# Optimization experiments

Hardware: AMD Instinct MI355X
Metric: run time of the kernel (lower is better)

The kernel has to match this reference:

```python
import jax, jax.numpy as jnp
import numpy as np

DIM_H = 128
HEADS = 8
HEAD_DIM = DIM_H // HEADS
N_NODES = 40000
N_EDGES = 640000
BN_EPS = 1e-5


def setup_inputs() -> dict:
    key = jax.random.key(0)
    ks = jax.random.split(key, 16)
    s = 0.05
    x = jax.random.normal(ks[0], (N_NODES, DIM_H), dtype=jnp.float32)
    edge_index = jax.random.randint(ks[1], (2, N_EDGES), 0, N_NODES, dtype=jnp.int64)
    p = lambda k, shp: jax.random.normal(k, shp, dtype=jnp.float32) * s
    return {
        "x": x,
        "edge_index": edge_index,
        "Wk": p(ks[2], (DIM_H, DIM_H)), "bk": p(ks[3], (DIM_H,)),
        "Wv": p(ks[4], (DIM_H, DIM_H)), "bv": p(ks[5], (DIM_H,)),
        "Wo": p(ks[6], (DIM_H, DIM_H)), "bo": p(ks[7], (DIM_H,)),
        "bn1_g": jnp.ones((DIM_H,), jnp.float32), "bn1_b": jnp.zeros((DIM_H,), jnp.float32),
        "W1": p(ks[8], (2 * DIM_H, DIM_H)), "b1": p(ks[9], (2 * DIM_H,)),
        "W2": p(ks[10], (DIM_H, 2 * DIM_H)), "b2": p(ks[11], (DIM_H,)),
        "bn2_g": jnp.ones((DIM_H,), jnp.float32), "bn2_b": jnp.zeros((DIM_H,), jnp.float32),
    }


def _batchnorm(h, gamma, beta):
    # BatchNorm1d in training mode: per-feature batch mean / biased var over nodes
    mu = jnp.mean(h, axis=0)
    var = jnp.mean((h - mu) ** 2, axis=0)
    return (h - mu) * jax.lax.rsqrt(var + BN_EPS) * gamma + beta


def _sparse_attn(x, edge_index, Wk, bk, Wv, bv, Wo, bo):
    N = x.shape[0]
    src, dst = edge_index[0], edge_index[1]
    K = (x @ Wk.T + bk).reshape(N, HEADS, HEAD_DIM)
    V = (x @ Wv.T + bv).reshape(N, HEADS, HEAD_DIM)
    Q = x.reshape(N, HEADS, HEAD_DIM)  # query is raw h (no projection)
    # per-edge scores [E, H]
    scores = jnp.sum(K[src] * Q[dst], axis=-1) / np.sqrt(HEAD_DIM).astype(np.float32)
    # segment softmax over destination nodes (pyg_softmax)
    m = jax.ops.segment_max(scores, dst, num_segments=N)
    e = jnp.exp(scores - m[dst])
    denom = jax.ops.segment_sum(e, dst, num_segments=N)
    attn = e / (denom[dst] + 1e-16)  # [E, H]
    messages = V[src] * attn[:, :, None]  # [E, H, D]
    out = jax.ops.segment_sum(messages, dst, num_segments=N)  # [N, H, D]
    return out.reshape(N, DIM_H) @ Wo.T + bo


def reference(x, edge_index, Wk, bk, Wv, bv, Wo, bo, bn1_g, bn1_b,
              W1, b1, W2, b2, bn2_g, bn2_b):
    h_attn = _sparse_attn(x, edge_index, Wk, bk, Wv, bv, Wo, bo)
    h = _batchnorm(x + h_attn, bn1_g, bn1_b)
    ff = jax.nn.relu(h @ W1.T + b1) @ W2.T + b2
    h = _batchnorm(h + ff, bn2_g, bn2_b)
    return h
```

## Files before the change

kernel.cpp:

```cpp
#include <hip/hip_runtime.h>

#define DIM 128
#define NSHARD 8

typedef __attribute__((ext_vector_type(2))) float f32x2;
typedef __attribute__((ext_vector_type(4))) _Float16 half4;
typedef __attribute__((ext_vector_type(8))) _Float16 half8;
typedef __attribute__((ext_vector_type(4))) float f32x4;

#define HP 136
#define UP 264

__device__ __forceinline__ unsigned char to_fp8(float v) {
  return (unsigned char)(__builtin_amdgcn_cvt_pk_fp8_f32(v, v, 0, false) & 0xff);
}

__global__ __launch_bounds__(256) void conv_wall(const float* __restrict__ Wk,
    const float* __restrict__ Wv, const float* __restrict__ Wo,
    const float* __restrict__ W1, const float* __restrict__ W2,
    _Float16* __restrict__ Wkh, _Float16* __restrict__ Wvh,
    _Float16* __restrict__ Woh, _Float16* __restrict__ W1h,
    _Float16* __restrict__ W2h, int* __restrict__ cnt, float* __restrict__ stats,
    int N) {
  int i = blockIdx.x * 256 + threadIdx.x;
  int nth = gridDim.x * 256;
  if (i < 16384) Wkh[i] = (_Float16)Wk[i];
  else if (i < 32768) Wvh[i - 16384] = (_Float16)Wv[i - 16384];
  else if (i < 49152) Woh[i - 32768] = (_Float16)Wo[i - 32768];
  else if (i < 81920) W1h[i - 49152] = (_Float16)W1[i - 49152];
  else if (i < 114688) W2h[i - 81920] = (_Float16)W2[i - 81920];
  for (int j = i; j < N * NSHARD; j += nth) cnt[j] = 0;
  if (i < 512) stats[i] = 0.f;
}

__global__ __launch_bounds__(256) void hist_rank(const int* __restrict__ ei,
    int* __restrict__ cnt, int* __restrict__ rank, int N, int E) {
  int e = blockIdx.x * 256 + threadIdx.x;
  if (e < E) rank[e] = atomicAdd(&cnt[(e & (NSHARD - 1)) * N + ei[E + e]], 1);
}

__global__ __launch_bounds__(256) void scanA(const int* __restrict__ cnt,
    int* __restrict__ rs, int* __restrict__ bsum, int N) {
  __shared__ int s[256];
  int t = threadIdx.x;
  int i = blockIdx.x * 256 + t;
  int v = 0;
  if (i < N)
#pragma unroll
    for (int sh = 0; sh < NSHARD; sh++) v += cnt[sh * N + i];
  s[t] = v;
  __syncthreads();
  for (int off = 1; off < 256; off <<= 1) {
    int add = (t >= off) ? s[t - off] : 0;
    __syncthreads();
    s[t] += add;
    __syncthreads();
  }
  if (i < N) rs[i] = s[t] - v;
  if (t == 255) bsum[blockIdx.x] = s[t];
}

__global__ __launch_bounds__(256) void scanBC(int* __restrict__ rs,
    const int* __restrict__ bsum, const int* __restrict__ cnt,
    int* __restrict__ rs_shard, int nblk, int N, int E) {
  __shared__ int s[256];
  __shared__ int ex[256];
  int t = threadIdx.x;
  int v = (t < nblk) ? bsum[t] : 0;
  s[t] = v;
  __syncthreads();
  for (int off = 1; off < 256; off <<= 1) {
    int add = (t >= off) ? s[t - off] : 0;
    __syncthreads();
    s[t] += add;
    __syncthreads();
  }
  ex[t] = s[t] - v;
  __syncthreads();
  int boff = ex[blockIdx.x];
  int i = blockIdx.x * 256 + t;
  if (i < N) {
    int b = rs[i] + boff;
    rs[i] = b;
#pragma unroll
    for (int sh = 0; sh < NSHARD; sh++) {
      rs_shard[sh * N + i] = b;
      b += cnt[sh * N + i];
    }
  }
  if (i == 0) rs[N] = E;
}

__global__ __launch_bounds__(256) void scatter_kv(const int* __restrict__ ei,
    const int* __restrict__ rs_shard, const int* __restrict__ rank,
    int* __restrict__ esrc, const float* __restrict__ x,
    const _Float16* __restrict__ Wkh, const float* __restrict__ bk,
    const _Float16* __restrict__ Wvh, const float* __restrict__ bv,
    unsigned char* __restrict__ KV8, int kvb, int N, int E) {
  __shared__ _Float16 xs[64 * HP];
  int tid = threadIdx.x;
  if ((int)blockIdx.x >= kvb) {
    int e = ((int)blockIdx.x - kvb) * 256 + tid;
    if (e < E)
      esrc[rs_shard[(e & (NSHARD - 1)) * N + ei[E + e]] + rank[e]] = ei[e];
    return;
  }
  int base = blockIdx.x * 64;
  int lane = tid & 63, w = tid >> 6;
  int l15 = lane & 15, quad = lane >> 4;

  for (int i = tid; i < 64 * 32; i += 256) {
    int m = i >> 5, c4 = i & 31;
    float4 tv = ((const float4*)x)[(size_t)(base + m) * 32 + c4];
    half4 hv;
    hv.x = (_Float16)tv.x; hv.y = (_Float16)tv.y;
    hv.z = (_Float16)tv.z; hv.w = (_Float16)tv.w;
    *(half4*)&xs[m * HP + c4 * 4] = hv;
  }
  __syncthreads();

  half8 afr[4][4];
#pragma unroll
  for (int mt = 0; mt < 4; mt++)
#pragma unroll
    for (int ks = 0; ks < 4; ks++)
      afr[mt][ks] = *(const half8*)&xs[(mt * 16 + l15) * HP + ks * 32 + quad * 8];

  const _Float16* W = (w < 2) ? Wkh : Wvh;
  const float* bias = (w < 2) ? bk : bv;
  int voff = (w < 2) ? 0 : 4;
  int c0 = (w & 1) * 64;

#pragma unroll
  for (int nt = 0; nt < 4; nt++) {
    int f = c0 + nt * 16 + l15;
    half8 bfr[4];
#pragma unroll
    for (int ks = 0; ks < 4; ks++)
      bfr[ks] = *(const half8*)&W[(size_t)f * 128 + ks * 32 + quad * 8];
    f32x4 acc[4];
#pragma unroll
    for (int mt = 0; mt < 4; mt++) acc[mt] = (f32x4){0.f, 0.f, 0.f, 0.f};
#pragma unroll
    for (int ks = 0; ks < 4; ks++)
#pragma unroll
      for (int mt = 0; mt < 4; mt++)
        acc[mt] = __builtin_amdgcn_mfma_f32_16x16x32_f16(afr[mt][ks], bfr[ks],
                                                          acc[mt], 0, 0, 0);
    float bb = bias[f];
    int fo = (f >> 2) * 8 + (f & 3) + voff;
#pragma unroll
    for (int mt = 0; mt < 4; mt++)
#pragma unroll
      for (int r = 0; r < 4; r++)
        KV8[(size_t)(base + mt * 16 + quad * 4 + r) * 256 + fo] =
            to_fp8(acc[mt][r] + bb);
  }
}

__global__ __launch_bounds__(256) void attn_agg(const unsigned char* __restrict__ KV8,
    const float* __restrict__ x, const int* __restrict__ rs,
    const int* __restrict__ esrc, _Float16* __restrict__ attn16, int N) {
  int wave = threadIdx.x >> 6, lane = threadIdx.x & 63;
  int n = blockIdx.x * 4 + wave;
  if (n >= N) return;
  int l = lane & 31, s = lane >> 5;
  float4 q = *(const float4*)&x[(size_t)n * DIM + 4 * l];
  int beg = rs[n], end = rs[n + 1];
  float a0 = 0.f, a1 = 0.f, a2 = 0.f, a3 = 0.f, dloc = 0.f;
  for (int e = beg + s; e < end; e += 8) {
    bool hh[4];
    int ss[4];
#pragma unroll
    for (int u = 0; u < 4; u++) hh[u] = (e + 2 * u) < end;
    ss[0] = esrc[e];
#pragma unroll
    for (int u = 1; u < 4; u++) ss[u] = hh[u] ? esrc[e + 2 * u] : ss[0];
    uint2 kv[4];
#pragma unroll
    for (int u = 0; u < 4; u++)
      kv[u] = *(const uint2*)&KV8[(size_t)ss[u] * 256 + 8 * l];
    float p[4];
#pragma unroll
    for (int u = 0; u < 4; u++) {
      f32x2 k01 = __builtin_amdgcn_cvt_pk_f32_fp8(kv[u].x, false);
      f32x2 k23 = __builtin_amdgcn_cvt_pk_f32_fp8(kv[u].x, true);
      p[u] = k01[0] * q.x + k01[1] * q.y + k23[0] * q.z + k23[1] * q.w;
    }
#pragma unroll
    for (int u = 0; u < 4; u++) p[u] += __shfl_xor(p[u], 1);
#pragma unroll
    for (int u = 0; u < 4; u++) p[u] += __shfl_xor(p[u], 2);
#pragma unroll
    for (int u = 0; u < 4; u++) {
      float ev = hh[u] ? __expf(p[u] * 0.25f) : 0.f;
      dloc += ev;
      f32x2 v01 = __builtin_amdgcn_cvt_pk_f32_fp8(kv[u].y, false);
      f32x2 v23 = __builtin_amdgcn_cvt_pk_f32_fp8(kv[u].y, true);
      a0 += ev * v01[0];
      a1 += ev * v01[1];
      a2 += ev * v23[0];
      a3 += ev * v23[1];
    }
  }
  dloc += __shfl_xor(dloc, 32);
  a0 += __shfl_xor(a0, 32);
  a1 += __shfl_xor(a1, 32);
  a2 += __shfl_xor(a2, 32);
  a3 += __shfl_xor(a3, 32);
  if (s == 0) {
    float inv = 1.0f / (dloc + 1e-16f);
    half4 o;
    o.x = (_Float16)(a0 * inv);
    o.y = (_Float16)(a1 * inv);
    o.z = (_Float16)(a2 * inv);
    o.w = (_Float16)(a3 * inv);
    *(half4*)&attn16[(size_t)n * DIM + 4 * l] = o;
  }
}

__global__ __launch_bounds__(512) void o_proj_mfma(const _Float16* __restrict__ attn16,
    const float* __restrict__ x, const _Float16* __restrict__ Woh,
    const float* __restrict__ bo, _Float16* __restrict__ t16,
    float* __restrict__ stats, int N) {
  __shared__ _Float16 as16[64 * HP];
  int tid = threadIdx.x;
  int base = blockIdx.x * 64;
  int lane = tid & 63, w = tid >> 6;
  int l15 = lane & 15, quad = lane >> 4;

  for (int i = tid; i < 64 * 16; i += 512) {
    int m = i >> 4, c8 = i & 15;
    *(half8*)&as16[m * HP + c8 * 8] =
        ((const half8*)attn16)[(size_t)(base + m) * 16 + c8];
  }
  __syncthreads();

  half8 afr[4][4];
#pragma unroll
  for (int mt = 0; mt < 4; mt++)
#pragma unroll
    for (int ks = 0; ks < 4; ks++)
      afr[mt][ks] = *(const half8*)&as16[(mt * 16 + l15) * HP + ks * 32 + quad * 8];

  int c0 = w * 16;
  f32x4 acc[4];
#pragma unroll
  for (int mt = 0; mt < 4; mt++) acc[mt] = (f32x4){0.f, 0.f, 0.f, 0.f};
#pragma unroll
  for (int ks = 0; ks < 4; ks++) {
    half8 b = *(const half8*)&Woh[(size_t)(c0 + l15) * 128 + ks * 32 + quad * 8];
#pragma unroll
    for (int mt = 0; mt < 4; mt++)
      acc[mt] = __builtin_amdgcn_mfma_f32_16x16x32_f16(afr[mt][ks], b, acc[mt],
                                                        0, 0, 0);
  }

  int f = c0 + l15;
  float bb = bo[f];
  float s = 0.f, q = 0.f;
#pragma unroll
  for (int mt = 0; mt < 4; mt++) {
#pragma unroll
    for (int r = 0; r < 4; r++) {
      int row = mt * 16 + quad * 4 + r;
      float tv = acc[mt][r] + bb + x[(size_t)(base + row) * DIM + f];
      t16[(size_t)(base + row) * DIM + f] = (_Float16)tv;
      s += tv;
      q += tv * tv;
    }
  }
  s += __shfl_xor(s, 16);
  s += __shfl_xor(s, 32);
  q += __shfl_xor(q, 16);
  q += __shfl_xor(q, 32);
  if (quad == 0) {
    atomicAdd(&stats[f], s);
    atomicAdd(&stats[128 + f], q);
  }
}

__global__ __launch_bounds__(512) void ffn_mfma(const _Float16* __restrict__ t16,
    const float* __restrict__ stats1, const float* __restrict__ g1,
    const float* __restrict__ bb1, const _Float16* __restrict__ W1h,
    const float* __restrict__ b1, const _Float16* __restrict__ W2h,
    const float* __restrict__ b2, _Float16* __restrict__ z16,
    float* __restrict__ stats2, float invN, int N) {
  __shared__ _Float16 hs[64 * HP];
  __shared__ _Float16 us[64 * UP];
  __shared__ float cf[256];
  int tid = threadIdx.x;
  int base = blockIdx.x * 64;
  int lane = tid & 63, w = tid >> 6;
  int l15 = lane & 15, quad = lane >> 4;

  if (tid < 128) {
    float mu = stats1[tid] * invN;
    float var = stats1[128 + tid] * invN - mu * mu;
    float a = rsqrtf(var + 1e-5f) * g1[tid];
    cf[tid] = a;
    cf[128 + tid] = bb1[tid] - mu * a;
  }
  __syncthreads();

  for (int i = tid; i < 64 * 16; i += 512) {
    int m = i >> 4, c8 = i & 15;
    half8 tv = ((const half8*)t16)[(size_t)(base + m) * 16 + c8];
    half8 hv;
#pragma unroll
    for (int j = 0; j < 8; j++) {
      int f = c8 * 8 + j;
      hv[j] = (_Float16)((float)tv[j] * cf[f] + cf[128 + f]);
    }
    *(half8*)&hs[m * HP + c8 * 8] = hv;
  }
  __syncthreads();

  int n0 = w * 32;
  half8 afr[4][4];
#pragma unroll
  for (int mt = 0; mt < 4; mt++)
#pragma unroll
    for (int ks = 0; ks < 4; ks++)
      afr[mt][ks] = *(const half8*)&hs[(mt * 16 + l15) * HP + ks * 32 + quad * 8];

#pragma unroll
  for (int nt = 0; nt < 2; nt++) {
    int n = n0 + nt * 16 + l15;
    half8 bfr[4];
#pragma unroll
    for (int ks = 0; ks < 4; ks++)
      bfr[ks] = *(const half8*)&W1h[(size_t)n * 128 + ks * 32 + quad * 8];
    f32x4 acc[4];
#pragma unroll
    for (int mt = 0; mt < 4; mt++) acc[mt] = (f32x4){0.f, 0.f, 0.f, 0.f};
#pragma unroll
    for (int ks = 0; ks < 4; ks++)
#pragma unroll
      for (int mt = 0; mt < 4; mt++)
        acc[mt] = __builtin_amdgcn_mfma_f32_16x16x32_f16(afr[mt][ks], bfr[ks],
                                                          acc[mt], 0, 0, 0);
    float bias = b1[n];
#pragma unroll
    for (int mt = 0; mt < 4; mt++)
#pragma unroll
      for (int r = 0; r < 4; r++)
        us[(mt * 16 + quad * 4 + r) * UP + n] =
            (_Float16)fmaxf(acc[mt][r] + bias, 0.f);
  }
  __syncthreads();

  int n2 = w * 16;
  f32x4 acc2[4];
#pragma unroll
  for (int mt = 0; mt < 4; mt++) acc2[mt] = (f32x4){0.f, 0.f, 0.f, 0.f};
  for (int ks = 0; ks < 8; ks++) {
    half8 a[4];
#pragma unroll
    for (int mt = 0; mt < 4; mt++)
      a[mt] = *(const half8*)&us[(mt * 16 + l15) * UP + ks * 32 + quad * 8];
    half8 b = *(const half8*)&W2h[(size_t)(n2 + l15) * 256 + ks * 32 + quad * 8];
#pragma unroll
    for (int mt = 0; mt < 4; mt++)
      acc2[mt] = __builtin_amdgcn_mfma_f32_16x16x32_f16(a[mt], b, acc2[mt],
                                                         0, 0, 0);
  }

  int f = n2 + l15;
  float bz = b2[f];
  float s = 0.f, q = 0.f;
#pragma unroll
  for (int mt = 0; mt < 4; mt++) {
#pragma unroll
    for (int r = 0; r < 4; r++) {
      int row = mt * 16 + quad * 4 + r;
      float hv = (float)hs[row * HP + f];
      float zv = hv + acc2[mt][r] + bz;
      z16[(size_t)(base + row) * DIM + f] = (_Float16)zv;
      s += zv;
      q += zv * zv;
    }
  }
  s += __shfl_xor(s, 16);
  s += __shfl_xor(s, 32);
  q += __shfl_xor(q, 16);
  q += __shfl_xor(q, 32);
  if (quad == 0) {
    atomicAdd(&stats2[f], s);
    atomicAdd(&stats2[128 + f], q);
  }
}

__global__ __launch_bounds__(256) void final_apply(const _Float16* __restrict__ z16,
    const float* __restrict__ stats2, const float* __restrict__ g2,
    const float* __restrict__ bb2, float* __restrict__ out, float invN,
    int total8) {
  __shared__ float cf[256];
  int tid = threadIdx.x;
  if (tid < 128) {
    float mu = stats2[tid] * invN;
    float var = stats2[128 + tid] * invN - mu * mu;
    float a = rsqrtf(var + 1e-5f) * g2[tid];
    cf[tid] = a;
    cf[128 + tid] = bb2[tid] - mu * a;
  }
  __syncthreads();
  int i = blockIdx.x * 256 + tid;
  if (i >= total8) return;
  int f0 = (i * 8) & 127;
  half8 zv = ((const half8*)z16)[i];
  float4 o1, o2;
  o1.x = (float)zv[0] * cf[f0 + 0] + cf[128 + f0 + 0];
  o1.y = (float)zv[1] * cf[f0 + 1] + cf[128 + f0 + 1];
  o1.z = (float)zv[2] * cf[f0 + 2] + cf[128 + f0 + 2];
  o1.w = (float)zv[3] * cf[f0 + 3] + cf[128 + f0 + 3];
  o2.x = (float)zv[4] * cf[f0 + 4] + cf[128 + f0 + 4];
  o2.y = (float)zv[5] * cf[f0 + 5] + cf[128 + f0 + 5];
  o2.z = (float)zv[6] * cf[f0 + 6] + cf[128 + f0 + 6];
  o2.w = (float)zv[7] * cf[f0 + 7] + cf[128 + f0 + 7];
  ((float4*)out)[2 * i] = o1;
  ((float4*)out)[2 * i + 1] = o2;
}

extern "C" void kernel_launch(void* const* d_in, const int* in_sizes, int n_in,
                              void* d_out, int out_size, void* d_ws, size_t ws_size,
                              hipStream_t stream) {
  const float* x = (const float*)d_in[0];
  const int* ei = (const int*)d_in[1];
  const float* Wk = (const float*)d_in[2];
  const float* bk = (const float*)d_in[3];
  const float* Wv = (const float*)d_in[4];
  const float* bv = (const float*)d_in[5];
  const float* Wo = (const float*)d_in[6];
  const float* bo = (const float*)d_in[7];
  const float* bn1_g = (const float*)d_in[8];
  const float* bn1_b = (const float*)d_in[9];
  const float* W1 = (const float*)d_in[10];
  const float* b1 = (const float*)d_in[11];
  const float* W2 = (const float*)d_in[12];
  const float* b2 = (const float*)d_in[13];
  const float* bn2_g = (const float*)d_in[14];
  const float* bn2_b = (const float*)d_in[15];
  float* out = (float*)d_out;

  int N = in_sizes[0] / DIM;
  int E = in_sizes[1] / 2;

  unsigned char* KV8 = (unsigned char*)d_ws;
  _Float16* attn16 = (_Float16*)(KV8 + (size_t)N * 256);
  _Float16* t16 = attn16 + (size_t)N * DIM;
  _Float16* z16 = t16 + (size_t)N * DIM;
  _Float16* W1h = z16 + (size_t)N * DIM;
  _Float16* W2h = W1h + 32768;
  _Float16* Wkh = W2h + 32768;
  _Float16* Wvh = Wkh + 16384;
  _Float16* Woh = Wvh + 16384;
  float* stats = (float*)(Woh + 16384);
  int* cnt = (int*)(stats + 512);
  int* rs = cnt + (size_t)N * NSHARD;
  int* rs_shard = rs + N + 1;
  int* rank = rs_shard + (size_t)N * NSHARD;
  int* esrc = rank + E;
  int* bsum = esrc + E;

  int nblk = (N + 255) / 256;
  int kvb = N / 64;
  int sblk = (E + 255) / 256;
  float invN = 1.0f / N;
  float* stats2 = stats + 256;

  conv_wall<<<512, 256, 0, stream>>>(Wk, Wv, Wo, W1, W2, Wkh, Wvh, Woh, W1h,
                                     W2h, cnt, stats, N);
  hist_rank<<<sblk, 256, 0, stream>>>(ei, cnt, rank, N, E);
  scanA<<<nblk, 256, 0, stream>>>(cnt, rs, bsum, N);
  scanBC<<<nblk, 256, 0, stream>>>(rs, bsum, cnt, rs_shard, nblk, N, E);
  scatter_kv<<<kvb + sblk, 256, 0, stream>>>(ei, rs_shard, rank, esrc, x, Wkh,
                                             bk, Wvh, bv, KV8, kvb, N, E);
  attn_agg<<<(N + 3) / 4, 256, 0, stream>>>(KV8, x, rs, esrc, attn16, N);
  o_proj_mfma<<<kvb, 512, 0, stream>>>(attn16, x, Woh, bo, t16, stats, N);
  ffn_mfma<<<kvb, 512, 0, stream>>>(t16, stats, bn1_g, bn1_b, W1h, b1, W2h, b2,
                                    z16, stats2, invN, N);
  final_apply<<<((N * DIM / 8) + 255) / 256, 256, 0, stream>>>(
      z16, stats2, bn2_g, bn2_b, out, invN, N * DIM / 8);
}
```

Measured before the change: 240.2 us.

## Regroup preprocessing kernels, use memset for zeroing, deepen attention edge unroll

Zeroing of stats and the shard counters moves to hipMemsetAsync, and weight conversion is fused with the histogram/rank pass into one launch. The KV projection now shares a launch with the first scan stage instead of the esrc scatter, which becomes its own kernel. The aim is fewer dependent launches and more overlap of independent work. The attention aggregation loop is unrolled from 4 to 8 edges per half-wave to keep more gathers in flight, at the cost of extra registers and more wasted iterations on low-degree nodes.

New measurement: 242.3 us. About the same (+0.9%).

```diff
diff --git a/kernel.cpp b/kernel.cpp
--- a/kernel.cpp
+++ b/kernel.cpp
@@ -15,49 +15,105 @@
   return (unsigned char)(__builtin_amdgcn_cvt_pk_fp8_f32(v, v, 0, false) & 0xff);
 }
 
-__global__ __launch_bounds__(256) void conv_wall(const float* __restrict__ Wk,
+__global__ __launch_bounds__(256) void conv_hist(const float* __restrict__ Wk,
     const float* __restrict__ Wv, const float* __restrict__ Wo,
     const float* __restrict__ W1, const float* __restrict__ W2,
     _Float16* __restrict__ Wkh, _Float16* __restrict__ Wvh,
     _Float16* __restrict__ Woh, _Float16* __restrict__ W1h,
-    _Float16* __restrict__ W2h, int* __restrict__ cnt, float* __restrict__ stats,
-    int N) {
-  int i = blockIdx.x * 256 + threadIdx.x;
-  int nth = gridDim.x * 256;
-  if (i < 16384) Wkh[i] = (_Float16)Wk[i];
-  else if (i < 32768) Wvh[i - 16384] = (_Float16)Wv[i - 16384];
-  else if (i < 49152) Woh[i - 32768] = (_Float16)Wo[i - 32768];
-  else if (i < 81920) W1h[i - 49152] = (_Float16)W1[i - 49152];
-  else if (i < 114688) W2h[i - 81920] = (_Float16)W2[i - 81920];
-  for (int j = i; j < N * NSHARD; j += nth) cnt[j] = 0;
-  if (i < 512) stats[i] = 0.f;
-}
-
-__global__ __launch_bounds__(256) void hist_rank(const int* __restrict__ ei,
+    _Float16* __restrict__ W2h, const int* __restrict__ ei,
     int* __restrict__ cnt, int* __restrict__ rank, int N, int E) {
-  int e = blockIdx.x * 256 + threadIdx.x;
-  if (e < E) rank[e] = atomicAdd(&cnt[(e & (NSHARD - 1)) * N + ei[E + e]], 1);
-}
-
-__global__ __launch_bounds__(256) void scanA(const int* __restrict__ cnt,
-    int* __restrict__ rs, int* __restrict__ bsum, int N) {
+  int tid = threadIdx.x;
+  if (blockIdx.x < 512) {
+    int i = blockIdx.x * 256 + tid;
+    if (i < 16384) Wkh[i] = (_Float16)Wk[i];
+    else if (i < 32768) Wvh[i - 16384] = (_Float16)Wv[i - 16384];
+    else if (i < 49152) Woh[i - 32768] = (_Float16)Wo[i - 32768];
+    else if (i < 81920) W1h[i - 49152] = (_Float16)W1[i - 49152];
+    else if (i < 114688) W2h[i - 81920] = (_Float16)W2[i - 81920];
+  } else {
+    int e = ((int)blockIdx.x - 512) * 256 + tid;
+    if (e < E) rank[e] = atomicAdd(&cnt[(e & (NSHARD - 1)) * N + ei[E + e]], 1);
+  }
+}
+
+__global__ __launch_bounds__(256) void scan_kv(const int* __restrict__ cnt,
+    int* __restrict__ rs, int* __restrict__ bsum, const float* __restrict__ x,
+    const _Float16* __restrict__ Wkh, const float* __restrict__ bk,
+    const _Float16* __restrict__ Wvh, const float* __restrict__ bv,
+    unsigned char* __restrict__ KV8, int nblk, int N) {
+  __shared__ _Float16 xs[64 * HP];
   __shared__ int s[256];
-  int t = threadIdx.x;
-  int i = blockIdx.x * 256 + t;
-  int v = 0;
-  if (i < N)
-#pragma unroll
-    for (int sh = 0; sh < NSHARD; sh++) v += cnt[sh * N + i];
-  s[t] = v;
-  __syncthreads();
-  for (int off = 1; off < 256; off <<= 1) {
-    int add = (t >= off) ? s[t - off] : 0;
+  int tid = threadIdx.x;
+  if ((int)blockIdx.x < nblk) {
+    int t = tid;
+    int i = blockIdx.x * 256 + t;
+    int v = 0;
+    if (i < N)
+#pragma unroll
+      for (int sh = 0; sh < NSHARD; sh++) v += cnt[sh * N + i];
+    s[t] = v;
     __syncthreads();
-    s[t] += add;
-    __syncthreads();
-  }
-  if (i < N) rs[i] = s[t] - v;
-  if (t == 255) bsum[blockIdx.x] = s[t];
+    for (int off = 1; off < 256; off <<= 1) {
+      int add = (t >= off) ? s[t - off] : 0;
+      __syncthreads();
+      s[t] += add;
+      __syncthreads();
+    }
+    if (i < N) rs[i] = s[t] - v;
+    if (t == 255) bsum[blockIdx.x] = s[t];
+    return;
+  }
+  int base = ((int)blockIdx.x - nblk) * 64;
+  int lane = tid & 63, w = tid >> 6;
+  int l15 = lane & 15, quad = lane >> 4;
+
+  for (int i = tid; i < 64 * 32; i += 256) {
+    int m = i >> 5, c4 = i & 31;
+    float4 tv = ((const float4*)x)[(size_t)(base + m) * 32 + c4];
+    half4 hv;
+    hv.x = (_Float16)tv.x; hv.y = (_Float16)tv.y;
+    hv.z = (_Float16)tv.z; hv.w = (_Float16)tv.w;
+    *(half4*)&xs[m * HP + c4 * 4] = hv;
+  }
+  __syncthreads();
+
+  half8 afr[4][4];
+#pragma unroll
+  for (int mt = 0; mt < 4; mt++)
+#pragma unroll
+    for (int ks = 0; ks < 4; ks++)
+      afr[mt][ks] = *(const half8*)&xs[(mt * 16 + l15) * HP + ks * 32 + quad * 8];
+
+  const _Float16* W = (w < 2) ? Wkh : Wvh;
+  const float* bias = (w < 2) ? bk : bv;
+  int voff = (w < 2) ? 0 : 4;
+  int c0 = (w & 1) * 64;
+
+#pragma unroll
+  for (int nt = 0; nt < 4; nt++) {
+    int f = c0 + nt * 16 + l15;
+    half8 bfr[4];
+#pragma unroll
+    for (int ks = 0; ks < 4; ks++)
+      bfr[ks] = *(const half8*)&W[(size_t)f * 128 + ks * 32 + quad * 8];
+    f32x4 acc[4];
+#pragma unroll
+    for (int mt = 0; mt < 4; mt++) acc[mt] = (f32x4){0.f, 0.f, 0.f, 0.f};
+#pragma unroll
+    for (int ks = 0; ks < 4; ks++)
+#pragma unroll
+      for (int mt = 0; mt < 4; mt++)
+        acc[mt] = __builtin_amdgcn_mfma_f32_16x16x32_f16(afr[mt][ks], bfr[ks],
+                                                          acc[mt], 0, 0, 0);
+    float bb = bias[f];
+    int fo = (f >> 2) * 8 + (f & 3) + voff;
+#pragma unroll
+    for (int mt = 0; mt < 4; mt++)
+#pragma unroll
+      for (int r = 0; r < 4; r++)
+        KV8[(size_t)(base + mt * 16 + quad * 4 + r) * 256 + fo] =
+            to_fp8(acc[mt][r] + bb);
+  }
 }
 
 __global__ __launch_bounds__(256) void scanBC(int* __restrict__ rs,
@@ -91,71 +147,12 @@
   if (i == 0) rs[N] = E;
 }
 
-__global__ __launch_bounds__(256) void scatter_kv(const int* __restrict__ ei,
+__global__ __launch_bounds__(256) void scatter2(const int* __restrict__ ei,
     const int* __restrict__ rs_shard, const int* __restrict__ rank,
-    int* __restrict__ esrc, const float* __restrict__ x,
-    const _Float16* __restrict__ Wkh, const float* __restrict__ bk,
-    const _Float16* __restrict__ Wvh, const float* __restrict__ bv,
-    unsigned char* __restrict__ KV8, int kvb, int N, int E) {
-  __shared__ _Float16 xs[64 * HP];
-  int tid = threadIdx.x;
-  if ((int)blockIdx.x >= kvb) {
-    int e = ((int)blockIdx.x - kvb) * 256 + tid;
-    if (e < E)
-      esrc[rs_shard[(e & (NSHARD - 1)) * N + ei[E + e]] + rank[e]] = ei[e];
-    return;
-  }
-  int base = blockIdx.x * 64;
-  int lane = tid & 63, w = tid >> 6;
-  int l15 = lane & 15, quad = lane >> 4;
-
-  for (int i = tid; i < 64 * 32; i += 256) {
-    int m = i >> 5, c4 = i & 31;
-    float4 tv = ((const float4*)x)[(size_t)(base + m) * 32 + c4];
-    half4 hv;
-    hv.x = (_Float16)tv.x; hv.y = (_Float16)tv.y;
-    hv.z = (_Float16)tv.z; hv.w = (_Float16)tv.w;
-    *(half4*)&xs[m * HP + c4 * 4] = hv;
-  }
-  __syncthreads();
-
-  half8 afr[4][4];
-#pragma unroll
-  for (int mt = 0; mt < 4; mt++)
-#pragma unroll
-    for (int ks = 0; ks < 4; ks++)
-      afr[mt][ks] = *(const half8*)&xs[(mt * 16 + l15) * HP + ks * 32 + quad * 8];
-
-  const _Float16* W = (w < 2) ? Wkh : Wvh;
-  const float* bias = (w < 2) ? bk : bv;
-  int voff = (w < 2) ? 0 : 4;
-  int c0 = (w & 1) * 64;
-
-#pragma unroll
-  for (int nt = 0; nt < 4; nt++) {
-    int f = c0 + nt * 16 + l15;
-    half8 bfr[4];
-#pragma unroll
-    for (int ks = 0; ks < 4; ks++)
-      bfr[ks] = *(const half8*)&W[(size_t)f * 128 + ks * 32 + quad * 8];
-    f32x4 acc[4];
-#pragma unroll
-    for (int mt = 0; mt < 4; mt++) acc[mt] = (f32x4){0.f, 0.f, 0.f, 0.f};
-#pragma unroll
-    for (int ks = 0; ks < 4; ks++)
-#pragma unroll
-      for (int mt = 0; mt < 4; mt++)
-        acc[mt] = __builtin_amdgcn_mfma_f32_16x16x32_f16(afr[mt][ks], bfr[ks],
-                                                          acc[mt], 0, 0, 0);
-    float bb = bias[f];
-    int fo = (f >> 2) * 8 + (f & 3) + voff;
-#pragma unroll
-    for (int mt = 0; mt < 4; mt++)
-#pragma unroll
-      for (int r = 0; r < 4; r++)
-        KV8[(size_t)(base + mt * 16 + quad * 4 + r) * 256 + fo] =
-            to_fp8(acc[mt][r] + bb);
-  }
+    int* __restrict__ esrc, int N, int E) {
+  int e = blockIdx.x * 256 + threadIdx.x;
+  if (e < E)
+    esrc[rs_shard[(e & (NSHARD - 1)) * N + ei[E + e]] + rank[e]] = ei[e];
 }
 
 __global__ __launch_bounds__(256) void attn_agg(const unsigned char* __restrict__ KV8,
@@ -168,31 +165,31 @@
   float4 q = *(const float4*)&x[(size_t)n * DIM + 4 * l];
   int beg = rs[n], end = rs[n + 1];
   float a0 = 0.f, a1 = 0.f, a2 = 0.f, a3 = 0.f, dloc = 0.f;
-  for (int e = beg + s; e < end; e += 8) {
-    bool hh[4];
-    int ss[4];
-#pragma unroll
-    for (int u = 0; u < 4; u++) hh[u] = (e + 2 * u) < end;
+  for (int e = beg + s; e < end; e += 16) {
+    bool hh[8];
+    int ss[8];
+#pragma unroll
+    for (int u = 0; u < 8; u++) hh[u] = (e + 2 * u) < end;
     ss[0] = esrc[e];
 #pragma unroll
-    for (int u = 1; u < 4; u++) ss[u] = hh[u] ? esrc[e + 2 * u] : ss[0];
-    uint2 kv[4];
-#pragma unroll
-    for (int u = 0; u < 4; u++)
+    for (int u = 1; u < 8; u++) ss[u] = hh[u] ? esrc[e + 2 * u] : ss[0];
+    uint2 kv[8];
+#pragma unroll
+    for (int u = 0; u < 8; u++)
       kv[u] = *(const uint2*)&KV8[(size_t)ss[u] * 256 + 8 * l];
-    float p[4];
-#pragma unroll
-    for (int u = 0; u < 4; u++) {
+    float p[8];
+#pragma unroll
+    for (int u = 0; u < 8; u++) {
       f32x2 k01 = __builtin_amdgcn_cvt_pk_f32_fp8(kv[u].x, false);
       f32x2 k23 = __builtin_amdgcn_cvt_pk_f32_fp8(kv[u].x, true);
       p[u] = k01[0] * q.x + k01[1] * q.y + k23[0] * q.z + k23[1] * q.w;
     }
 #pragma unroll
-    for (int u = 0; u < 4; u++) p[u] += __shfl_xor(p[u], 1);
-#pragma unroll
-    for (int u = 0; u < 4; u++) p[u] += __shfl_xor(p[u], 2);
-#pragma unroll
-    for (int u = 0; u < 4; u++) {
+    for (int u = 0; u < 8; u++) p[u] += __shfl_xor(p[u], 1);
+#pragma unroll
+    for (int u = 0; u < 8; u++) p[u] += __shfl_xor(p[u], 2);
+#pragma unroll
+    for (int u = 0; u < 8; u++) {
       float ev = hh[u] ? __expf(p[u] * 0.25f) : 0.f;
       dloc += ev;
       f32x2 v01 = __builtin_amdgcn_cvt_pk_f32_fp8(kv[u].y, false);
@@ -469,13 +466,13 @@
   float invN = 1.0f / N;
   float* stats2 = stats + 256;
 
-  conv_wall<<<512, 256, 0, stream>>>(Wk, Wv, Wo, W1, W2, Wkh, Wvh, Woh, W1h,
-                                     W2h, cnt, stats, N);
-  hist_rank<<<sblk, 256, 0, stream>>>(ei, cnt, rank, N, E);
-  scanA<<<nblk, 256, 0, stream>>>(cnt, rs, bsum, N);
+  hipMemsetAsync(stats, 0, (512 + (size_t)N * NSHARD) * 4, stream);
+  conv_hist<<<512 + sblk, 256, 0, stream>>>(Wk, Wv, Wo, W1, W2, Wkh, Wvh, Woh,
+                                            W1h, W2h, ei, cnt, rank, N, E);
+  scan_kv<<<nblk + kvb, 256, 0, stream>>>(cnt, rs, bsum, x, Wkh, bk, Wvh, bv,
+                                          KV8, nblk, N);
   scanBC<<<nblk, 256, 0, stream>>>(rs, bsum, cnt, rs_shard, nblk, N, E);
-  scatter_kv<<<kvb + sblk, 256, 0, stream>>>(ei, rs_shard, rank, esrc, x, Wkh,
-                                             bk, Wvh, bv, KV8, kvb, N, E);
+  scatter2<<<sblk, 256, 0, stream>>>(ei, rs_shard, rank, esrc, N, E);
   attn_agg<<<(N + 3) / 4, 256, 0, stream>>>(KV8, x, rs, esrc, attn16, N);
   o_proj_mfma<<<kvb, 512, 0, stream>>>(attn16, x, Woh, bo, t16, stats, N);
   ffn_mfma<<<kvb, 512, 0, stream>>>(t16, stats, bn1_g, bn1_b, W1h, b1, W2h, b2,
```

## Widen attention gather to 16-byte loads and cache fp16 copy of x

Applied to the files above, without the earlier changes.

The attention aggregation kernel now has each lane handle 8 channels with 16-byte KV loads instead of 4 channels with 8-byte loads. It processes 4 edges per wave step instead of 2, and one shuffle-reduction stage is removed. scatter_kv also writes an fp16 copy of x, which the attention query and the o_proj residual read in place of fp32 x, halving those reads. This adds an extra N×128 fp16 write and lowers the precision of the residual add.

After: 242.8 us. No clear change (+1.1%).

```diff
diff --git a/kernel.cpp b/kernel.cpp
--- a/kernel.cpp
+++ b/kernel.cpp
@@ -96,7 +96,8 @@
     int* __restrict__ esrc, const float* __restrict__ x,
     const _Float16* __restrict__ Wkh, const float* __restrict__ bk,
     const _Float16* __restrict__ Wvh, const float* __restrict__ bv,
-    unsigned char* __restrict__ KV8, int kvb, int N, int E) {
+    unsigned char* __restrict__ KV8, _Float16* __restrict__ x16,
+    int kvb, int N, int E) {
   __shared__ _Float16 xs[64 * HP];
   int tid = threadIdx.x;
   if ((int)blockIdx.x >= kvb) {
@@ -116,6 +117,7 @@
     hv.x = (_Float16)tv.x; hv.y = (_Float16)tv.y;
     hv.z = (_Float16)tv.z; hv.w = (_Float16)tv.w;
     *(half4*)&xs[m * HP + c4 * 4] = hv;
+    *(half4*)&x16[(size_t)(base + m) * DIM + c4 * 4] = hv;
   }
   __syncthreads();
 
@@ -159,68 +161,79 @@
 }
 
 __global__ __launch_bounds__(256) void attn_agg(const unsigned char* __restrict__ KV8,
-    const float* __restrict__ x, const int* __restrict__ rs,
+    const _Float16* __restrict__ x16, const int* __restrict__ rs,
     const int* __restrict__ esrc, _Float16* __restrict__ attn16, int N) {
   int wave = threadIdx.x >> 6, lane = threadIdx.x & 63;
   int n = blockIdx.x * 4 + wave;
   if (n >= N) return;
-  int l = lane & 31, s = lane >> 5;
-  float4 q = *(const float4*)&x[(size_t)n * DIM + 4 * l];
+  int c = lane & 15, h = lane >> 4;
+  half8 qh = *(const half8*)&x16[(size_t)n * DIM + 8 * c];
+  float q0 = (float)qh[0], q1 = (float)qh[1], q2 = (float)qh[2],
+        q3 = (float)qh[3], q4 = (float)qh[4], q5 = (float)qh[5],
+        q6 = (float)qh[6], q7 = (float)qh[7];
   int beg = rs[n], end = rs[n + 1];
-  float a0 = 0.f, a1 = 0.f, a2 = 0.f, a3 = 0.f, dloc = 0.f;
-  for (int e = beg + s; e < end; e += 8) {
+  float a0 = 0.f, a1 = 0.f, a2 = 0.f, a3 = 0.f;
+  float a4 = 0.f, a5 = 0.f, a6 = 0.f, a7 = 0.f, dloc = 0.f;
+  for (int e = beg + h; e < end; e += 16) {
     bool hh[4];
     int ss[4];
 #pragma unroll
-    for (int u = 0; u < 4; u++) hh[u] = (e + 2 * u) < end;
+    for (int u = 0; u < 4; u++) hh[u] = (e + 4 * u) < end;
     ss[0] = esrc[e];
 #pragma unroll
-    for (int u = 1; u < 4; u++) ss[u] = hh[u] ? esrc[e + 2 * u] : ss[0];
-    uint2 kv[4];
+    for (int u = 1; u < 4; u++) ss[u] = hh[u] ? esrc[e + 4 * u] : ss[0];
+    uint4 kv[4];
 #pragma unroll
     for (int u = 0; u < 4; u++)
-      kv[u] = *(const uint2*)&KV8[(size_t)ss[u] * 256 + 8 * l];
+      kv[u] = *(const uint4*)&KV8[(size_t)ss[u] * 256 + 16 * c];
     float p[4];
 #pragma unroll
     for (int u = 0; u < 4; u++) {
       f32x2 k01 = __builtin_amdgcn_cvt_pk_f32_fp8(kv[u].x, false);
       f32x2 k23 = __builtin_amdgcn_cvt_pk_f32_fp8(kv[u].x, true);
-      p[u] = k01[0] * q.x + k01[1] * q.y + k23[0] * q.z + k23[1] * q.w;
+      f32x2 k45 = __builtin_amdgcn_cvt_pk_f32_fp8(kv[u].z, false);
+      f32x2 k67 = __builtin_amdgcn_cvt_pk_f32_fp8(kv[u].z, true);
+      p[u] = k01[0] * q0 + k01[1] * q1 + k23[0] * q2 + k23[1] * q3 +
+             k45[0] * q4 + k45[1] * q5 + k67[0] * q6 + k67[1] * q7;
     }
 #pragma unroll
     for (int u = 0; u < 4; u++) p[u] += __shfl_xor(p[u], 1);
-#pragma unroll
-    for (int u = 0; u < 4; u++) p[u] += __shfl_xor(p[u], 2);
 #pragma unroll
     for (int u = 0; u < 4; u++) {
       float ev = hh[u] ? __expf(p[u] * 0.25f) : 0.f;
       dloc += ev;
       f32x2 v01 = __builtin_amdgcn_cvt_pk_f32_fp8(kv[u].y, false);
       f32x2 v23 = __builtin_amdgcn_cvt_pk_f32_fp8(kv[u].y, true);
-      a0 += ev * v01[0];
-      a1 += ev * v01[1];
-      a2 += ev * v23[0];
-      a3 += ev * v23[1];
-    }
-  }
-  dloc += __shfl_xor(dloc, 32);
-  a0 += __shfl_xor(a0, 32);
-  a1 += __shfl_xor(a1, 32);
-  a2 += __shfl_xor(a2, 32);
-  a3 += __shfl_xor(a3, 32);
-  if (s == 0) {
+      f32x2 v45 = __builtin_amdgcn_cvt_pk_f32_fp8(kv[u].w, false);
+      f32x2 v67 = __builtin_amdgcn_cvt_pk_f32_fp8(kv[u].w, true);
+      a0 += ev * v01[0]; a1 += ev * v01[1];
+      a2 += ev * v23[0]; a3 += ev * v23[1];
+      a4 += ev * v45[0]; a5 += ev * v45[1];
+      a6 += ev * v67[0]; a7 += ev * v67[1];
+    }
+  }
+  dloc += __shfl_xor(dloc, 16); dloc += __shfl_xor(dloc, 32);
+  a0 += __shfl_xor(a0, 16); a0 += __shfl_xor(a0, 32);
+  a1 += __shfl_xor(a1, 16); a1 += __shfl_xor(a1, 32);
+  a2 += __shfl_xor(a2, 16); a2 += __shfl_xor(a2, 32);
+  a3 += __shfl_xor(a3, 16); a3 += __shfl_xor(a3, 32);
+  a4 += __shfl_xor(a4, 16); a4 += __shfl_xor(a4, 32);
+  a5 += __shfl_xor(a5, 16); a5 += __shfl_xor(a5, 32);
+  a6 += __shfl_xor(a6, 16); a6 += __shfl_xor(a6, 32);
+  a7 += __shfl_xor(a7, 16); a7 += __shfl_xor(a7, 32);
+  if (h == 0) {
     float inv = 1.0f / (dloc + 1e-16f);
-    half4 o;
-    o.x = (_Float16)(a0 * inv);
-    o.y = (_Float16)(a1 * inv);
-    o.z = (_Float16)(a2 * inv);
-    o.w = (_Float16)(a3 * inv);
-    *(half4*)&attn16[(size_t)n * DIM + 4 * l] = o;
+    half8 o;
+    o[0] = (_Float16)(a0 * inv); o[1] = (_Float16)(a1 * inv);
+    o[2] = (_Float16)(a2 * inv); o[3] = (_Float16)(a3 * inv);
+    o[4] = (_Float16)(a4 * inv); o[5] = (_Float16)(a5 * inv);
+    o[6] = (_Float16)(a6 * inv); o[7] = (_Float16)(a7 * inv);
+    *(half8*)&attn16[(size_t)n * DIM + 8 * c] = o;
   }
 }
 
 __global__ __launch_bounds__(512) void o_proj_mfma(const _Float16* __restrict__ attn16,
-    const float* __restrict__ x, const _Float16* __restrict__ Woh,
+    const _Float16* __restrict__ x16, const _Float16* __restrict__ Woh,
     const float* __restrict__ bo, _Float16* __restrict__ t16,
     float* __restrict__ stats, int N) {
   __shared__ _Float16 as16[64 * HP];
@@ -264,7 +277,7 @@
 #pragma unroll
     for (int r = 0; r < 4; r++) {
       int row = mt * 16 + quad * 4 + r;
-      float tv = acc[mt][r] + bb + x[(size_t)(base + row) * DIM + f];
+      float tv = acc[mt][r] + bb + (float)x16[(size_t)(base + row) * DIM + f];
       t16[(size_t)(base + row) * DIM + f] = (_Float16)tv;
       s += tv;
       q += tv * tv;
@@ -450,7 +463,8 @@
   _Float16* attn16 = (_Float16*)(KV8 + (size_t)N * 256);
   _Float16* t16 = attn16 + (size_t)N * DIM;
   _Float16* z16 = t16 + (size_t)N * DIM;
-  _Float16* W1h = z16 + (size_t)N * DIM;
+  _Float16* x16 = z16 + (size_t)N * DIM;
+  _Float16* W1h = x16 + (size_t)N * DIM;
   _Float16* W2h = W1h + 32768;
   _Float16* Wkh = W2h + 32768;
   _Float16* Wvh = Wkh + 16384;
@@ -475,9 +489,9 @@
   scanA<<<nblk, 256, 0, stream>>>(cnt, rs, bsum, N);
   scanBC<<<nblk, 256, 0, stream>>>(rs, bsum, cnt, rs_shard, nblk, N, E);
   scatter_kv<<<kvb + sblk, 256, 0, stream>>>(ei, rs_shard, rank, esrc, x, Wkh,
-                                             bk, Wvh, bv, KV8, kvb, N, E);
-  attn_agg<<<(N + 3) / 4, 256, 0, stream>>>(KV8, x, rs, esrc, attn16, N);
-  o_proj_mfma<<<kvb, 512, 0, stream>>>(attn16, x, Woh, bo, t16, stats, N);
+                                             bk, Wvh, bv, KV8, x16, kvb, N, E);
+  attn_agg<<<(N + 3) / 4, 256, 0, stream>>>(KV8, x16, rs, esrc, attn16, N);
+  o_proj_mfma<<<kvb, 512, 0, stream>>>(attn16, x16, Woh, bo, t16, stats, N);
   ffn_mfma<<<kvb, 512, 0, stream>>>(t16, stats, bn1_g, bn1_b, W1h, b1, W2h, b2,
                                     z16, stats2, invN, N);
   final_apply<<<((N * DIM / 8) + 255) / 256, 256, 0, stream>>>(
```
